# Kernel tuning notes

Hardware: AMD Instinct MI355X
Metric: run time of the kernel (lower is better)

## Reference

```python
import jax, jax.numpy as jnp
import numpy as np

N_NODES = 100000
N_EDGES = 3200000
IN_CH = 384
HID = 128

def _gcn_layer(x, src, dst, norm, W, b, n_nodes):
    # PyG GCNConv: h = x @ W; out[dst] += norm * h[src]; out += b
    h = x @ W                                   # [N, out_ch]
    msg = h[src] * norm[:, None]                 # [E+N, out_ch] gather + scale
    out = jax.ops.segment_sum(msg, dst, num_segments=n_nodes)
    return out + b

def setup_inputs() -> dict:
    key = jax.random.key(0)
    k = jax.random.split(key, 7)
    x = jax.random.normal(k[0], (N_NODES, IN_CH), dtype=jnp.float32)
    edge_index = jax.random.randint(k[1], (2, N_EDGES), 0, N_NODES, dtype=jnp.int64)
    # Glorot-style init for GCN weights, zeros for biases (PyG default)
    W1 = jax.random.normal(k[2], (IN_CH, HID), dtype=jnp.float32) / np.sqrt(IN_CH)
    b1 = jnp.zeros((HID,), dtype=jnp.float32)
    W2 = jax.random.normal(k[3], (HID, HID), dtype=jnp.float32) / np.sqrt(HID)
    b2 = jnp.zeros((HID,), dtype=jnp.float32)
    return {"x": x, "edge_index": edge_index, "W1": W1, "b1": b1, "W2": W2, "b2": b2}

def reference(x, edge_index, W1, b1, W2, b2):
    n_nodes = x.shape[0]
    # GCNConv default: add self-loops, symmetric normalization D^-1/2 A D^-1/2
    loop = jnp.arange(n_nodes, dtype=edge_index.dtype)
    src = jnp.concatenate([edge_index[0], loop])   # [E+N]
    dst = jnp.concatenate([edge_index[1], loop])   # [E+N]
    deg = jax.ops.segment_sum(jnp.ones_like(dst, dtype=x.dtype), dst, num_segments=n_nodes)
    deg_inv_sqrt = jnp.where(deg > 0, jax.lax.rsqrt(jnp.maximum(deg, 1.0)), 0.0)
    norm = deg_inv_sqrt[src] * deg_inv_sqrt[dst]   # [E+N]
    h = _gcn_layer(x, src, dst, norm, W1, b1, n_nodes)
    h = jax.nn.relu(h)                              # dropout is identity in eval mode
    out = _gcn_layer(h, src, dst, norm, W2, b2, n_nodes)
    return out
```

## Files before the change

kernel.cpp:

```cpp
#include <hip/hip_runtime.h>

#define N_NODES 100000
#define N_EDGES 3200000
#define IN_CH   384
#define HID     128
#define BKT_SHIFT 7
#define NBKT ((N_NODES + 127) >> 7)
#define BINBLK 256
#define BTHREADS 512
#define CHUNK4 (N_EDGES / 4 / BINBLK)

typedef __attribute__((ext_vector_type(8))) short          bf16x8;
typedef __attribute__((ext_vector_type(8))) unsigned short u16x8;
typedef __attribute__((ext_vector_type(4))) float          f32x4;

static __device__ __forceinline__ unsigned short f2bf(float f) {
    unsigned u = __float_as_uint(f);
    unsigned r = (u + 0x7fffu + ((u >> 16) & 1u)) >> 16;
    return (unsigned short)r;
}

__global__ void k_wt2(const float* __restrict__ W1, const float* __restrict__ W2,
                      unsigned short* __restrict__ wt1, unsigned short* __restrict__ wt2) {
    int i = blockIdx.x * blockDim.x + threadIdx.x;
    if (i < IN_CH * 128) {
        int k = i >> 7, n = i & 127;
        wt1[(size_t)n * IN_CH + k] = f2bf(W1[i]);
    } else if (i < (IN_CH + HID) * 128) {
        int j = i - IN_CH * 128;
        int k = j >> 7, n = j & 127;
        wt2[(size_t)n * HID + k] = f2bf(W2[j]);
    }
}

__global__ __launch_bounds__(BTHREADS) void k_bhist(const int* __restrict__ dst,
                                                    unsigned* __restrict__ hist) {
    __shared__ unsigned lh[NBKT];
    for (int i = threadIdx.x; i < NBKT; i += BTHREADS) lh[i] = 0;
    __syncthreads();
    const int4* d4 = (const int4*)dst;
    const int base = blockIdx.x * CHUNK4;
    for (int i = threadIdx.x; i < CHUNK4; i += BTHREADS) {
        int4 v = d4[base + i];
        atomicAdd(&lh[v.x >> BKT_SHIFT], 1u);
        atomicAdd(&lh[v.y >> BKT_SHIFT], 1u);
        atomicAdd(&lh[v.z >> BKT_SHIFT], 1u);
        atomicAdd(&lh[v.w >> BKT_SHIFT], 1u);
    }
    __syncthreads();
    for (int i = threadIdx.x; i < NBKT; i += BTHREADS) hist[i * BINBLK + blockIdx.x] = lh[i];
}

__global__ __launch_bounds__(BINBLK) void k_bscan(unsigned* __restrict__ hist,
                                                  unsigned* __restrict__ bintot) {
    __shared__ unsigned s[BINBLK];
    const int b = blockIdx.x, t = threadIdx.x;
    unsigned v = hist[b * BINBLK + t];
    s[t] = v;
    __syncthreads();
    for (int off = 1; off < BINBLK; off <<= 1) {
        unsigned x = s[t];
        unsigned y = (t >= off) ? s[t - off] : 0u;
        __syncthreads();
        s[t] = x + y;
        __syncthreads();
    }
    hist[b * BINBLK + t] = s[t] - v;
    if (t == BINBLK - 1) bintot[b] = s[BINBLK - 1];
}

__global__ __launch_bounds__(1024) void k_gs(const unsigned* __restrict__ bintot,
                                             unsigned* __restrict__ B2, int n, int E) {
    __shared__ unsigned s[1024];
    const int t = threadIdx.x;
    unsigned v = (t < n) ? bintot[t] : 0u;
    s[t] = v;
    __syncthreads();
    for (int off = 1; off < 1024; off <<= 1) {
        unsigned x = s[t];
        unsigned y = (t >= off) ? s[t - off] : 0u;
        __syncthreads();
        s[t] = x + y;
        __syncthreads();
    }
    if (t < n) B2[t] = s[t] - v;
    if (t == 0) B2[n] = (unsigned)E;
}

__global__ __launch_bounds__(BTHREADS) void k_bscat(const int* __restrict__ src,
                                                    const int* __restrict__ dst,
                                                    const unsigned* __restrict__ hist,
                                                    const unsigned* __restrict__ B2,
                                                    unsigned* __restrict__ ebuf) {
    __shared__ unsigned lcur[NBKT];
    for (int i = threadIdx.x; i < NBKT; i += BTHREADS)
        lcur[i] = B2[i] + hist[i * BINBLK + blockIdx.x];
    __syncthreads();
    const int4* s4 = (const int4*)src;
    const int4* d4 = (const int4*)dst;
    const int base = blockIdx.x * CHUNK4;
    for (int i = threadIdx.x; i < CHUNK4; i += BTHREADS) {
        int4 sv = s4[base + i];
        int4 dv = d4[base + i];
        unsigned p;
        p = atomicAdd(&lcur[dv.x >> BKT_SHIFT], 1u);
        ebuf[p] = ((unsigned)(dv.x & 127) << 17) | (unsigned)sv.x;
        p = atomicAdd(&lcur[dv.y >> BKT_SHIFT], 1u);
        ebuf[p] = ((unsigned)(dv.y & 127) << 17) | (unsigned)sv.y;
        p = atomicAdd(&lcur[dv.z >> BKT_SHIFT], 1u);
        ebuf[p] = ((unsigned)(dv.z & 127) << 17) | (unsigned)sv.z;
        p = atomicAdd(&lcur[dv.w >> BKT_SHIFT], 1u);
        ebuf[p] = ((unsigned)(dv.w & 127) << 17) | (unsigned)sv.w;
    }
}

__global__ __launch_bounds__(BTHREADS) void k_fill(const unsigned* __restrict__ ebuf,
                                                   const unsigned* __restrict__ B2,
                                                   unsigned* __restrict__ rowptr,
                                                   float* __restrict__ dis,
                                                   int* __restrict__ csr, int N, int E) {
    __shared__ unsigned lcnt[128];
    __shared__ unsigned lcur[128];
    const int b = blockIdx.x, t = threadIdx.x;
    const int n0 = b << BKT_SHIFT;
    const int cnt = min(128, N - n0);
    if (t < 128) lcnt[t] = 0;
    __syncthreads();
    const unsigned beg = B2[b], end = B2[b + 1];
    for (unsigned i = beg + t; i < end; i += BTHREADS)
        atomicAdd(&lcnt[ebuf[i] >> 17], 1u);
    __syncthreads();
    unsigned deg_t = (t < 128) ? lcnt[t] : 0u;
    if (t < 128) lcur[t] = deg_t;
    __syncthreads();
    for (int off = 1; off < 128; off <<= 1) {
        unsigned x = 0;
        if (t < 128) {
            x = lcur[t];
            if (t >= off) x += lcur[t - off];
        }
        __syncthreads();
        if (t < 128) lcur[t] = x;
        __syncthreads();
    }
    if (t < cnt) {
        unsigned ex = beg + lcur[t] - deg_t;
        rowptr[n0 + t] = ex;
        dis[n0 + t] = rsqrtf((float)(deg_t + 1u));
        lcur[t] = ex;
    }
    if (b == (int)gridDim.x - 1 && t == 0) rowptr[N] = (unsigned)E;
    __syncthreads();
    for (unsigned i = beg + t; i < end; i += BTHREADS) {
        unsigned v = ebuf[i];
        unsigned pos = atomicAdd(&lcur[v >> 17], 1u);
        csr[pos] = (int)(v & 0x1FFFFu);
    }
}

template<bool AF32>
__global__ __launch_bounds__(256) void k_gemm_mfma(const void* __restrict__ Ap,
                                                   const unsigned short* __restrict__ Wt,
                                                   const float* __restrict__ dis,
                                                   unsigned short* __restrict__ C,
                                                   int M, int K) {
    __shared__ unsigned short As[128][40];
    __shared__ unsigned short Bs[128][40];
    const int tid = threadIdx.x;
    const int w = tid >> 6;
    const int l = tid & 63;
    const int row0 = blockIdx.x * 128;

    f32x4 acc[2][8];
#pragma unroll
    for (int i = 0; i < 2; i++)
#pragma unroll
        for (int f = 0; f < 8; f++) acc[i][f] = (f32x4){0.f, 0.f, 0.f, 0.f};

    for (int k0 = 0; k0 < K; k0 += 32) {
#pragma unroll
        for (int t = 0; t < 2; t++) {
            int g = tid + t * 256;
            int r = g >> 2, k8 = (g & 3) * 8;
            int ar = row0 + r;
            u16x8 u = {0, 0, 0, 0, 0, 0, 0, 0};
            if (AF32) {
                if (ar < M) {
                    const float* ap = (const float*)Ap + (size_t)ar * K + k0 + k8;
                    float4 v0 = *(const float4*)ap;
                    float4 v1 = *(const float4*)(ap + 4);
                    u[0] = f2bf(v0.x); u[1] = f2bf(v0.y); u[2] = f2bf(v0.z); u[3] = f2bf(v0.w);
                    u[4] = f2bf(v1.x); u[5] = f2bf(v1.y); u[6] = f2bf(v1.z); u[7] = f2bf(v1.w);
                }
            } else {
                if (ar < M)
                    u = *(const u16x8*)((const unsigned short*)Ap + (size_t)ar * K + k0 + k8);
            }
            *(u16x8*)&As[r][k8] = u;
        }
#pragma unroll
        for (int t = 0; t < 2; t++) {
            int g = tid + t * 256;
            int n = g >> 2, k8 = (g & 3) * 8;
            *(u16x8*)&Bs[n][k8] = *(const u16x8*)&Wt[(size_t)n * K + k0 + k8];
        }
        __syncthreads();

        bf16x8 a0 = *(const bf16x8*)&As[w * 32 + (l & 15)][(l >> 4) * 8];
        bf16x8 a1 = *(const bf16x8*)&As[w * 32 + 16 + (l & 15)][(l >> 4) * 8];
#pragma unroll
        for (int f = 0; f < 8; f++) {
            bf16x8 bfr = *(const bf16x8*)&Bs[f * 16 + (l & 15)][(l >> 4) * 8];
            acc[0][f] = __builtin_amdgcn_mfma_f32_16x16x32_bf16(a0, bfr, acc[0][f], 0, 0, 0);
            acc[1][f] = __builtin_amdgcn_mfma_f32_16x16x32_bf16(a1, bfr, acc[1][f], 0, 0, 0);
        }
        __syncthreads();
    }

    const int colb = l & 15;
    const int rowq = (l >> 4) * 4;
#pragma unroll
    for (int i = 0; i < 2; i++)
#pragma unroll
        for (int r = 0; r < 4; r++) {
            int row = row0 + w * 32 + i * 16 + rowq + r;
            if (row < M) {
                float dv = dis[row];
#pragma unroll
                for (int f = 0; f < 8; f++)
                    C[(size_t)row * 128 + f * 16 + colb] = f2bf(dv * acc[i][f][r]);
            }
        }
}

template<int RELU, int OUTBF>
__global__ __launch_bounds__(256) void k_aggregate(const unsigned short* __restrict__ h,
                                                   const int* __restrict__ csr_src,
                                                   const unsigned* __restrict__ rowptr,
                                                   const float* __restrict__ dis,
                                                   const float* __restrict__ bias,
                                                   void* __restrict__ outp, int N) {
    const int wid = (int)((blockIdx.x * (blockDim.x >> 6)) + (threadIdx.x >> 6));
    const int d = __builtin_amdgcn_readfirstlane(wid);
    if (d >= N) return;
    const int lane = threadIdx.x & 63;
    const unsigned beg = rowptr[d], end = rowptr[d + 1];
    const float dd = dis[d];
    const unsigned* h1 = reinterpret_cast<const unsigned*>(h);

    unsigned hv = h1[(size_t)d * 64 + lane];
    float ax = __uint_as_float(hv << 16);
    float ay = __uint_as_float(hv & 0xffff0000u);

    unsigned e = beg;
    for (; e + 8 <= end; e += 8) {
        int s[8];
        unsigned v[8];
#pragma unroll
        for (int u = 0; u < 8; u++) s[u] = csr_src[e + u];
#pragma unroll
        for (int u = 0; u < 8; u++) v[u] = h1[(size_t)s[u] * 64 + lane];
#pragma unroll
        for (int u = 0; u < 8; u++) {
            ax += __uint_as_float(v[u] << 16);
            ay += __uint_as_float(v[u] & 0xffff0000u);
        }
    }
    for (; e < end; e++) {
        int s0 = csr_src[e];
        unsigned v0 = h1[(size_t)s0 * 64 + lane];
        ax += __uint_as_float(v0 << 16);
        ay += __uint_as_float(v0 & 0xffff0000u);
    }
    float2 bv = reinterpret_cast<const float2*>(bias)[lane];
    float r0 = fmaf(dd, ax, bv.x);
    float r1 = fmaf(dd, ay, bv.y);
    if (RELU) { r0 = fmaxf(r0, 0.f); r1 = fmaxf(r1, 0.f); }
    if (OUTBF) {
        unsigned pack = (unsigned)f2bf(r0) | ((unsigned)f2bf(r1) << 16);
        reinterpret_cast<unsigned*>(outp)[(size_t)d * 64 + lane] = pack;
    } else {
        reinterpret_cast<float2*>(outp)[(size_t)d * 64 + lane] = make_float2(r0, r1);
    }
}

extern "C" void kernel_launch(void* const* d_in, const int* in_sizes, int n_in,
                              void* d_out, int out_size, void* d_ws, size_t ws_size,
                              hipStream_t stream) {
    const float* x  = (const float*)d_in[0];
    const int*   ei = (const int*)d_in[1];
    const float* W1 = (const float*)d_in[2];
    const float* b1 = (const float*)d_in[3];
    const float* W2 = (const float*)d_in[4];
    const float* b2 = (const float*)d_in[5];
    const int* src = ei;
    const int* dst = ei + N_EDGES;
    float* out = (float*)d_out;

    char* ws = (char*)d_ws;
    float*          dis    = (float*)ws;
    unsigned*       rowptr = (unsigned*)(ws + 400128);
    unsigned*       B2     = (unsigned*)(ws + 800256);
    unsigned*       bintot = (unsigned*)(ws + 803584);
    unsigned short* wt1    = (unsigned short*)(ws + 806912);
    unsigned short* wt2    = (unsigned short*)(ws + 905216);
    unsigned*       hist   = (unsigned*)(ws + 937984);
    unsigned*       ebuf   = (unsigned*)(ws + 1738880);
    int*            csr    = (int*)(ws + 14538880);
    unsigned short* hbf    = (unsigned short*)(ws + 27338880);
    unsigned short* abf    = (unsigned short*)(ws + 52938880);

    k_wt2<<<((IN_CH + HID) * 128 + 255) / 256, 256, 0, stream>>>(W1, W2, wt1, wt2);

    k_bhist<<<BINBLK, BTHREADS, 0, stream>>>(dst, hist);
    k_bscan<<<NBKT, BINBLK, 0, stream>>>(hist, bintot);
    k_gs<<<1, 1024, 0, stream>>>(bintot, B2, NBKT, N_EDGES);
    k_bscat<<<BINBLK, BTHREADS, 0, stream>>>(src, dst, hist, B2, ebuf);
    k_fill<<<NBKT, BTHREADS, 0, stream>>>(ebuf, B2, rowptr, dis, csr, N_NODES, N_EDGES);

    k_gemm_mfma<true><<<(N_NODES + 127) / 128, 256, 0, stream>>>(x, wt1, dis, hbf, N_NODES, IN_CH);
    k_aggregate<1, 1><<<(N_NODES * 64 + 255) / 256, 256, 0, stream>>>(hbf, csr, rowptr, dis, b1, abf, N_NODES);

    k_gemm_mfma<false><<<(N_NODES + 127) / 128, 256, 0, stream>>>(abf, wt2, dis, hbf, N_NODES, HID);
    k_aggregate<0, 0><<<(N_NODES * 64 + 255) / 256, 256, 0, stream>>>(hbf, csr, rowptr, dis, b2, out, N_NODES);
}
```

Baseline: 382.6 us.

## Store hidden features in column-planar layout and aggregate per feature plane

The GEMM now writes its bf16 output as 8 planes of 16 columns, each plane [N,16], and the second GEMM reads its input in that layout. The aggregation kernel is rewritten so each block handles one 16-column plane for 32 destination nodes. Each wave spreads 8 edges across lane groups and combines them with shuffle reductions. The aim is to shrink the gathered working set per pass so it fits in cache better, at the cost of reading each edge list 8 times and adding reduction overhead.

```diff
diff --git a/kernel.cpp b/kernel.cpp
--- a/kernel.cpp
+++ b/kernel.cpp
@@ -193,8 +193,12 @@
                     u[4] = f2bf(v1.x); u[5] = f2bf(v1.y); u[6] = f2bf(v1.z); u[7] = f2bf(v1.w);
                 }
             } else {
-                if (ar < M)
-                    u = *(const u16x8*)((const unsigned short*)Ap + (size_t)ar * K + k0 + k8);
+                if (ar < M) {
+                    int kk = k0 + k8;
+                    int p = kk >> 4, rem = kk & 15;
+                    u = *(const u16x8*)((const unsigned short*)Ap +
+                                        ((size_t)p * M + ar) * 16 + rem);
+                }
             }
             *(u16x8*)&As[r][k8] = u;
         }
@@ -228,59 +232,59 @@
                 float dv = dis[row];
 #pragma unroll
                 for (int f = 0; f < 8; f++)
-                    C[(size_t)row * 128 + f * 16 + colb] = f2bf(dv * acc[i][f][r]);
+                    C[((size_t)f * M + row) * 16 + colb] = f2bf(dv * acc[i][f][r]);
             }
         }
 }
 
 template<int RELU, int OUTBF>
-__global__ __launch_bounds__(256) void k_aggregate(const unsigned short* __restrict__ h,
-                                                   const int* __restrict__ csr_src,
-                                                   const unsigned* __restrict__ rowptr,
-                                                   const float* __restrict__ dis,
-                                                   const float* __restrict__ bias,
-                                                   void* __restrict__ outp, int N) {
-    const int wid = (int)((blockIdx.x * (blockDim.x >> 6)) + (threadIdx.x >> 6));
-    const int d = __builtin_amdgcn_readfirstlane(wid);
-    if (d >= N) return;
-    const int lane = threadIdx.x & 63;
-    const unsigned beg = rowptr[d], end = rowptr[d + 1];
-    const float dd = dis[d];
-    const unsigned* h1 = reinterpret_cast<const unsigned*>(h);
-
-    unsigned hv = h1[(size_t)d * 64 + lane];
-    float ax = __uint_as_float(hv << 16);
-    float ay = __uint_as_float(hv & 0xffff0000u);
-
-    unsigned e = beg;
-    for (; e + 8 <= end; e += 8) {
-        int s[8];
-        unsigned v[8];
-#pragma unroll
-        for (int u = 0; u < 8; u++) s[u] = csr_src[e + u];
-#pragma unroll
-        for (int u = 0; u < 8; u++) v[u] = h1[(size_t)s[u] * 64 + lane];
-#pragma unroll
-        for (int u = 0; u < 8; u++) {
-            ax += __uint_as_float(v[u] << 16);
-            ay += __uint_as_float(v[u] & 0xffff0000u);
-        }
-    }
-    for (; e < end; e++) {
-        int s0 = csr_src[e];
-        unsigned v0 = h1[(size_t)s0 * 64 + lane];
-        ax += __uint_as_float(v0 << 16);
-        ay += __uint_as_float(v0 & 0xffff0000u);
-    }
-    float2 bv = reinterpret_cast<const float2*>(bias)[lane];
-    float r0 = fmaf(dd, ax, bv.x);
-    float r1 = fmaf(dd, ay, bv.y);
-    if (RELU) { r0 = fmaxf(r0, 0.f); r1 = fmaxf(r1, 0.f); }
-    if (OUTBF) {
-        unsigned pack = (unsigned)f2bf(r0) | ((unsigned)f2bf(r1) << 16);
-        reinterpret_cast<unsigned*>(outp)[(size_t)d * 64 + lane] = pack;
-    } else {
-        reinterpret_cast<float2*>(outp)[(size_t)d * 64 + lane] = make_float2(r0, r1);
+__global__ __launch_bounds__(256) void k_agg_pl(const unsigned* __restrict__ hp,
+                                                const int* __restrict__ csr,
+                                                const unsigned* __restrict__ rowptr,
+                                                const float* __restrict__ dis,
+                                                const float* __restrict__ bias,
+                                                void* __restrict__ outp, int N) {
+    const int g  = blockIdx.x & 7;
+    const int nb = blockIdx.x >> 3;
+    const int wv = threadIdx.x >> 6;
+    const int l  = threadIdx.x & 63;
+    const int es = l >> 3;
+    const int j  = l & 7;
+    const unsigned* plane = hp + (size_t)g * N * 8;
+    const float2 bv = reinterpret_cast<const float2*>(bias)[g * 8 + j];
+
+#pragma unroll 1
+    for (int q = 0; q < 8; q++) {
+        const int d = nb * 32 + wv * 8 + q;
+        const unsigned beg = rowptr[d], end = rowptr[d + 1];
+        const float dd = dis[d];
+        float ax = 0.f, ay = 0.f;
+        for (unsigned e = beg + es; ; e += 8) {
+            bool valid = (e < end);
+            if (!__any(valid)) break;
+            int s = valid ? csr[e] : 0;
+            unsigned w = valid ? plane[(size_t)s * 8 + j] : 0u;
+            ax += __uint_as_float(w << 16);
+            ay += __uint_as_float(w & 0xffff0000u);
+        }
+        ax += __shfl_xor(ax, 8);  ay += __shfl_xor(ay, 8);
+        ax += __shfl_xor(ax, 16); ay += __shfl_xor(ay, 16);
+        ax += __shfl_xor(ax, 32); ay += __shfl_xor(ay, 32);
+        unsigned wsf = plane[(size_t)d * 8 + j];
+        ax += __uint_as_float(wsf << 16);
+        ay += __uint_as_float(wsf & 0xffff0000u);
+        float r0 = fmaf(dd, ax, bv.x);
+        float r1 = fmaf(dd, ay, bv.y);
+        if (RELU) { r0 = fmaxf(r0, 0.f); r1 = fmaxf(r1, 0.f); }
+        if (es == 0) {
+            if (OUTBF) {
+                reinterpret_cast<unsigned*>(outp)[((size_t)g * N + d) * 8 + j] =
+                    (unsigned)f2bf(r0) | ((unsigned)f2bf(r1) << 16);
+            } else {
+                reinterpret_cast<float2*>(outp)[(size_t)d * 64 + g * 8 + j] =
+                    make_float2(r0, r1);
+            }
+        }
     }
 }
 
@@ -318,9 +322,11 @@
     k_bscat<<<BINBLK, BTHREADS, 0, stream>>>(src, dst, hist, B2, ebuf);
     k_fill<<<NBKT, BTHREADS, 0, stream>>>(ebuf, B2, rowptr, dis, csr, N_NODES, N_EDGES);
 
+    const int AGG_GRID = (N_NODES / 32) * 8;
+
     k_gemm_mfma<true><<<(N_NODES + 127) / 128, 256, 0, stream>>>(x, wt1, dis, hbf, N_NODES, IN_CH);
-    k_aggregate<1, 1><<<(N_NODES * 64 + 255) / 256, 256, 0, stream>>>(hbf, csr, rowptr, dis, b1, abf, N_NODES);
+    k_agg_pl<1, 1><<<AGG_GRID, 256, 0, stream>>>((const unsigned*)hbf, csr, rowptr, dis, b1, abf, N_NODES);
 
     k_gemm_mfma<false><<<(N_NODES + 127) / 128, 256, 0, stream>>>(abf, wt2, dis, hbf, N_NODES, HID);
-    k_aggregate<0, 0><<<(N_NODES * 64 + 255) / 256, 256, 0, stream>>>(hbf, csr, rowptr, dis, b2, out, N_NODES);
-}
+    k_agg_pl<0, 0><<<AGG_GRID, 256, 0, stream>>>((const unsigned*)hbf, csr, rowptr, dis, b2, out, N_NODES);
+}
```

Result: slower. 813.5 us (+112.6%).
